# Optimization experiments

Hardware: AMD Instinct MI355X
Metric: run time of the kernel (lower is better)

## Reference

```python
import jax, jax.numpy as jnp
from jax import lax
import numpy as np

# label LUT: 36 raw labels -> 20 classes (from the module's labmap dict)
LUT = jnp.array(list(range(20)) + [1,2,3,4,5,6,7,8,9,10,14,15,16,17,18,19], dtype=jnp.int32)
R = 20  # kernel radius = ceil(truncated(4) * max sigma(5)); static for jit


def _gauss_kernel(sigma):
    k = jnp.arange(-R, R + 1, dtype=jnp.float32)
    w = jnp.exp(-0.5 * (k / sigma) ** 2)
    return w / jnp.sum(w)


def _smooth_axis(vol, w, axis):
    # vol: [D,H,W]; separable 1D zero-padded convolution along `axis`
    v = jnp.moveaxis(vol, axis, -1)
    sh = v.shape
    v2 = v.reshape(-1, 1, sh[-1])                      # [N,1,L]
    out = lax.conv_general_dilated(v2, w.reshape(1, 1, -1), (1,), [(R, R)])
    return jnp.moveaxis(out.reshape(sh), -1, axis)


def _gsmooth3(vol, sigma):
    # vol: [D,H,W]
    w = _gauss_kernel(sigma)
    for ax in range(3):
        vol = _smooth_axis(vol, w, ax)
    return vol


def setup_inputs() -> dict:
    key = jax.random.key(0)
    ks = jax.random.split(key, 6)
    shape = (1, 128, 160, 128)
    x = jax.random.randint(ks[0], shape, 0, 36, dtype=jnp.int32)
    noise = jax.random.normal(ks[1], (20,) + shape, dtype=jnp.float32)
    mus = jax.random.uniform(ks[2], (20,), minval=0.0, maxval=255.0, dtype=jnp.float32)
    stds = jax.random.uniform(ks[3], (20,), minval=0.0, maxval=16.0, dtype=jnp.float32)
    gmm_sigmas = jax.random.uniform(ks[4], (20,), minval=0.1, maxval=5.0, dtype=jnp.float32)
    final_sigma = jax.random.uniform(ks[5], (), minval=0.1, maxval=5.0, dtype=jnp.float32)
    return {"x": x, "noise": noise, "mus": mus, "stds": stds,
            "gmm_sigmas": gmm_sigmas, "final_sigma": final_sigma}


def reference(x, noise, mus, stds, gmm_sigmas, final_sigma):
    # 1) vectorized LUT remap (replaces the sequential tensor.apply_)
    xr = LUT[x[0]]                                      # [D,H,W] int32
    # 2) per-class masked Gaussian noise fields: (mu_i + std_i * N(0,1)) * (xr == i)
    classes = jnp.arange(20, dtype=jnp.int32)
    masks = (xr[None] == classes[:, None, None, None]).astype(jnp.float32)  # [20,D,H,W]
    fields = (mus[:, None, None, None] + stds[:, None, None, None] * noise[:, 0]) * masks
    # 3) per-class Gaussian smoothing (vmapped over the 20 classes), then sum
    smoothed = jax.vmap(_gsmooth3)(fields, gmm_sigmas)  # [20,D,H,W]
    summed = jnp.sum(smoothed, axis=0)                  # [D,H,W]
    # 4) final Gaussian smooth
    out = _gsmooth3(summed, final_sigma)
    return out[None]                                    # [1,D,H,W]
```

## Files before the change

kernel.cpp:

```cpp
#include <hip/hip_runtime.h>

constexpr int DD = 128, HH = 160, WW = 128;
constexpr int ZSTR = HH * WW;
constexpr long long NV = (long long)DD * HH * WW;
constexpr long long VOLB = NV * 4;
constexpr int RAD = 20, NTAP = 41;
constexpr int PW = 176;
constexpr int PADC = 24;
constexpr long long NVP = (long long)DD * HH * PW;

__device__ __forceinline__ int lutmap(int v) {
    return v < 20 ? v : (v < 30 ? v - 19 : v - 16);
}

__device__ __forceinline__ void taps(const float* win, const float* __restrict__ w,
                                     float acc[8]) {
#pragma unroll
    for (int k = 0; k < NTAP; ++k) {
        float wk = w[k];
#pragma unroll
        for (int p = 0; p < 8; ++p) acc[p] = fmaf(wk, win[k + p], acc[p]);
    }
}

__global__ __launch_bounds__(256) void kprep2(const int* __restrict__ x,
                                              const float* __restrict__ noise,
                                              const float* __restrict__ mus,
                                              const float* __restrict__ stds,
                                              float* __restrict__ vp,
                                              unsigned char* __restrict__ cp) {
    int z = blockIdx.y;
    int idx = blockIdx.x * 256 + threadIdx.x;
    int y = idx / PW, xp = idx - y * PW;
    long long po = (long long)z * HH * PW + idx;
    int gx = xp - PADC;
    if ((unsigned)gx < (unsigned)WW) {
        long long gi = (long long)z * ZSTR + (long long)y * WW + gx;
        int c = lutmap(x[gi]);
        vp[po] = mus[c] + stds[c] * noise[(long long)c * NV + gi];
        cp[po] = (unsigned char)c;
    } else {
        vp[po] = 0.f;
        cp[po] = (unsigned char)255;
    }
}

__global__ __launch_bounds__(256) void kpad(const float* __restrict__ src,
                                            float* __restrict__ vp) {
    int z = blockIdx.y;
    int idx = blockIdx.x * 256 + threadIdx.x;
    int y = idx / PW, xp = idx - y * PW;
    long long po = (long long)z * HH * PW + idx;
    int gx = xp - PADC;
    vp[po] = ((unsigned)gx < (unsigned)WW)
                 ? src[(long long)z * ZSTR + (long long)y * WW + gx]
                 : 0.f;
}

__global__ void kweights(const float* __restrict__ gsig, const float* __restrict__ fsig,
                         float* __restrict__ wts) {
    int c = threadIdx.x;
    if (c > 20) return;
    float sigma = (c < 20) ? gsig[c] : fsig[0];
    float inv = 1.0f / sigma;
    float buf[NTAP];
    float s = 0.f;
    for (int k = 0; k < NTAP; ++k) {
        float d = (float)(k - RAD) * inv;
        buf[k] = expf(-0.5f * d * d);
        s += buf[k];
    }
    float r = 1.0f / s;
    for (int k = 0; k < NTAP; ++k) wts[c * NTAP + k] = buf[k] * r;
}

template <bool MASKED>
__global__ __launch_bounds__(256, 4) void ksmooth_xy2(const float* __restrict__ vp,
                                                      const unsigned char* __restrict__ cp,
                                                      const float* __restrict__ wts,
                                                      float* __restrict__ dst, int c0) {
    __shared__ float A2[208][33];

    const int cls_i = MASKED ? (c0 + (int)blockIdx.x) : 20;
    const int x0 = (int)blockIdx.y * 32;
    const int z = blockIdx.z;
    const float* __restrict__ w = wts + cls_i * NTAP;
    const int tid = threadIdx.x;

    for (int i = tid; i < 48 * 32; i += 256) {
        int r = i >> 5, xx = i & 31;
        A2[(r < 24) ? r : (160 + r)][xx] = 0.f;
    }

    const long long zb = (long long)z * HH * PW;
    const int m = tid & 3, q = tid >> 2, xb = m * 8;
#pragma unroll
    for (int pass = 0; pass < 3; ++pass) {
        int y = pass * 64 + q;
        if (y < HH) {
            const float* srcp = vp + zb + (long long)y * PW + (x0 + xb + 4);
            float win[48];
            if (MASKED) {
                const unsigned* cu =
                    (const unsigned*)(cp + zb + (long long)y * PW + (x0 + xb + 4));
                const unsigned cb = (unsigned)cls_i;
#pragma unroll
                for (int i = 0; i < 12; ++i) {
                    float4 v4 = ((const float4*)srcp)[i];
                    unsigned u = cu[i];
                    win[4 * i + 0] = ((u & 0xffu) == cb) ? v4.x : 0.f;
                    win[4 * i + 1] = (((u >> 8) & 0xffu) == cb) ? v4.y : 0.f;
                    win[4 * i + 2] = (((u >> 16) & 0xffu) == cb) ? v4.z : 0.f;
                    win[4 * i + 3] = ((u >> 24) == cb) ? v4.w : 0.f;
                }
            } else {
#pragma unroll
                for (int i = 0; i < 12; ++i) {
                    float4 v4 = ((const float4*)srcp)[i];
                    win[4 * i + 0] = v4.x;
                    win[4 * i + 1] = v4.y;
                    win[4 * i + 2] = v4.z;
                    win[4 * i + 3] = v4.w;
                }
            }
            float acc[8] = {0, 0, 0, 0, 0, 0, 0, 0};
            taps(win, w, acc);
#pragma unroll
            for (int p = 0; p < 8; ++p) A2[24 + y][xb + p] = acc[p];
        }
    }
    __syncthreads();

    const int x = tid & 31, yg = tid >> 5;
    const long long obase =
        (MASKED ? ((long long)blockIdx.x * DD + z) : (long long)z) * ZSTR;
#pragma unroll
    for (int pass = 0; pass < 3; ++pass) {
        int yb = pass * 64 + yg * 8;
        if (yb < HH) {
            float win[48];
#pragma unroll
            for (int j = 0; j < 48; ++j) win[j] = A2[yb + 4 + j][x];
            float acc[8] = {0, 0, 0, 0, 0, 0, 0, 0};
            taps(win, w, acc);
#pragma unroll
            for (int p = 0; p < 8; ++p)
                dst[obase + (long long)(yb + p) * WW + x0 + x] = acc[p];
        }
    }
}

template <bool ACCUM>
__global__ __launch_bounds__(256) void ksmooth_z(const float* __restrict__ src,
                                                 const float* __restrict__ wts,
                                                 float* __restrict__ out, int c0,
                                                 int nc) {
    constexpr int LW = 33;
    __shared__ float L[104 * LW];

    const int x0 = blockIdx.x * 32;
    const int z0 = blockIdx.y * 64;
    const int y = blockIdx.z;
    const int x = threadIdx.x & 31;
    const int tg = threadIdx.x >> 5;

    float acc[8] = {0, 0, 0, 0, 0, 0, 0, 0};
    for (int cc = 0; cc < nc; ++cc) {
        const float* w = wts + (ACCUM ? (c0 + cc) : 20) * NTAP;
        const float* sv = src + (long long)cc * NV;
        for (int t = tg; t < 104; t += 8) {
            int gz = z0 - RAD + t;
            float v = ((unsigned)gz < (unsigned)DD)
                          ? sv[(long long)gz * ZSTR + (long long)y * WW + x0 + x]
                          : 0.f;
            L[t * LW + x] = v;
        }
        __syncthreads();
        {
            const int zb2 = tg * 8;
            float win[48];
#pragma unroll
            for (int j = 0; j < 48; ++j) win[j] = L[(zb2 + j) * LW + x];
            taps(win, w, acc);
        }
        __syncthreads();
    }
    const int zb2 = tg * 8;
#pragma unroll
    for (int p = 0; p < 8; ++p) {
        long long o = (long long)(z0 + zb2 + p) * ZSTR + (long long)y * WW + x0 + x;
        if (ACCUM)
            out[o] += acc[p];
        else
            out[o] = acc[p];
    }
}

extern "C" void kernel_launch(void* const* d_in, const int* in_sizes, int n_in,
                              void* d_out, int out_size, void* d_ws, size_t ws_size,
                              hipStream_t stream) {
    const int* x = (const int*)d_in[0];
    const float* noise = (const float*)d_in[1];
    const float* mus = (const float*)d_in[2];
    const float* stds = (const float*)d_in[3];
    const float* gsig = (const float*)d_in[4];
    const float* fsig = (const float*)d_in[5];
    float* out = (float*)d_out;

    char* ws = (char*)d_ws;
    size_t off = 0;
    float* wts = (float*)(ws + off);
    off += 4096;
    float* vp = (float*)(ws + off);
    off += (size_t)(NVP * 4);
    unsigned char* cpv = (unsigned char*)(ws + off);
    off += (size_t)NVP;
    float* xy = (float*)(ws + off);
    float* ftmp = xy;

    long long cap = ((long long)ws_size - (long long)off) / VOLB;
    int C = cap < 1 ? 1 : (cap > 20 ? 20 : (int)cap);

    kweights<<<1, 64, 0, stream>>>(gsig, fsig, wts);
    kprep2<<<dim3(HH * PW / 256, DD), 256, 0, stream>>>(x, noise, mus, stds, vp, cpv);
    hipMemsetAsync(d_out, 0, (size_t)VOLB, stream);

    for (int c0 = 0; c0 < 20; c0 += C) {
        int cc = (20 - c0) < C ? (20 - c0) : C;
        ksmooth_xy2<true><<<dim3(cc, 4, DD), 256, 0, stream>>>(vp, cpv, wts, xy, c0);
        ksmooth_z<true><<<dim3(4, 2, HH), 256, 0, stream>>>(xy, wts, out, c0, cc);
    }
    kpad<<<dim3(HH * PW / 256, DD), 256, 0, stream>>>(out, vp);
    ksmooth_xy2<false><<<dim3(1, 4, DD), 256, 0, stream>>>(vp, cpv, wts, ftmp, 0);
    ksmooth_z<false><<<dim3(4, 2, HH), 256, 0, stream>>>(ftmp, wts, out, 0, 1);
}
```

Measured before the change: 572.4 us.

## Rewrite z-smoothing with full-depth tiles, float4 loads and double-buffered class prefetch

The z-axis smoothing kernel now gives each block a 16-wide column spanning all 128 z slices, instead of a 32-wide column covering 64 z. This removes the 40-slice halo reload and the per-element bounds checks; the zero halos are written to shared memory once. Global loads become float4, and the next class's slab is prefetched into registers and written to a second shared buffer while the current class is convolved, dropping one barrier per class. The cost is larger shared-memory use per block, which may lower occupancy, and narrower 16-float output rows.

```diff
diff --git a/kernel.cpp b/kernel.cpp
--- a/kernel.cpp
+++ b/kernel.cpp
@@ -151,44 +151,81 @@
 }
 
 template <bool ACCUM>
-__global__ __launch_bounds__(256) void ksmooth_z(const float* __restrict__ src,
-                                                 const float* __restrict__ wts,
-                                                 float* __restrict__ out, int c0,
-                                                 int nc) {
-    constexpr int LW = 33;
-    __shared__ float L[104 * LW];
-
-    const int x0 = blockIdx.x * 32;
-    const int z0 = blockIdx.y * 64;
-    const int y = blockIdx.z;
-    const int x = threadIdx.x & 31;
-    const int tg = threadIdx.x >> 5;
+__global__ __launch_bounds__(256) void ksmooth_z3(const float* __restrict__ src,
+                                                  const float* __restrict__ wts,
+                                                  float* __restrict__ out, int c0,
+                                                  int nc) {
+    __shared__ float L[2][168][17];
+
+    const int x0 = (int)blockIdx.x * 16;
+    const int y = (int)blockIdx.y;
+    const int tid = threadIdx.x;
+    const int sxq = tid & 3;
+    const int szr = tid >> 2;
+    const int cx = tid & 15;
+    const int tg = tid >> 4;
+    const int zb = tg * 8;
+
+    const long long colbase = (long long)y * WW + x0;
+    const long long sgoff = colbase + sxq * 4;
+
+    for (int i = tid; i < 2 * 40 * 16; i += 256) {
+        int b = i / 640;
+        int rem = i - b * 640;
+        int r = rem >> 4, col = rem & 15;
+        L[b][(r < 20) ? r : (128 + r)][col] = 0.f;
+    }
+
+    {
+        const float4 va = *(const float4*)(src + (long long)szr * ZSTR + sgoff);
+        const float4 vb = *(const float4*)(src + (long long)(szr + 64) * ZSTR + sgoff);
+        const int wc = sxq * 4;
+        L[0][20 + szr][wc + 0] = va.x;
+        L[0][20 + szr][wc + 1] = va.y;
+        L[0][20 + szr][wc + 2] = va.z;
+        L[0][20 + szr][wc + 3] = va.w;
+        L[0][84 + szr][wc + 0] = vb.x;
+        L[0][84 + szr][wc + 1] = vb.y;
+        L[0][84 + szr][wc + 2] = vb.z;
+        L[0][84 + szr][wc + 3] = vb.w;
+    }
+    __syncthreads();
 
     float acc[8] = {0, 0, 0, 0, 0, 0, 0, 0};
     for (int cc = 0; cc < nc; ++cc) {
-        const float* w = wts + (ACCUM ? (c0 + cc) : 20) * NTAP;
-        const float* sv = src + (long long)cc * NV;
-        for (int t = tg; t < 104; t += 8) {
-            int gz = z0 - RAD + t;
-            float v = ((unsigned)gz < (unsigned)DD)
-                          ? sv[(long long)gz * ZSTR + (long long)y * WW + x0 + x]
-                          : 0.f;
-            L[t * LW + x] = v;
+        const int cur = cc & 1;
+        const bool more = (cc + 1 < nc);
+        float4 na, nb;
+        if (more) {
+            const float* sv = src + (long long)(cc + 1) * NV;
+            na = *(const float4*)(sv + (long long)szr * ZSTR + sgoff);
+            nb = *(const float4*)(sv + (long long)(szr + 64) * ZSTR + sgoff);
+        }
+        {
+            const float* w = wts + (ACCUM ? (c0 + cc) : 20) * NTAP;
+            float win[48];
+#pragma unroll
+            for (int j = 0; j < 48; ++j) win[j] = L[cur][zb + j][cx];
+            taps(win, w, acc);
+        }
+        if (more) {
+            const int nxt = cur ^ 1;
+            const int wc = sxq * 4;
+            L[nxt][20 + szr][wc + 0] = na.x;
+            L[nxt][20 + szr][wc + 1] = na.y;
+            L[nxt][20 + szr][wc + 2] = na.z;
+            L[nxt][20 + szr][wc + 3] = na.w;
+            L[nxt][84 + szr][wc + 0] = nb.x;
+            L[nxt][84 + szr][wc + 1] = nb.y;
+            L[nxt][84 + szr][wc + 2] = nb.z;
+            L[nxt][84 + szr][wc + 3] = nb.w;
         }
         __syncthreads();
-        {
-            const int zb2 = tg * 8;
-            float win[48];
-#pragma unroll
-            for (int j = 0; j < 48; ++j) win[j] = L[(zb2 + j) * LW + x];
-            taps(win, w, acc);
-        }
-        __syncthreads();
-    }
-    const int zb2 = tg * 8;
+    }
+
 #pragma unroll
     for (int p = 0; p < 8; ++p) {
-        long long o = (long long)(z0 + zb2 + p) * ZSTR + (long long)y * WW + x0 + x;
+        long long o = (long long)(zb + p) * ZSTR + colbase + cx;
         if (ACCUM)
             out[o] += acc[p];
         else
@@ -228,9 +265,9 @@
     for (int c0 = 0; c0 < 20; c0 += C) {
         int cc = (20 - c0) < C ? (20 - c0) : C;
         ksmooth_xy2<true><<<dim3(cc, 4, DD), 256, 0, stream>>>(vp, cpv, wts, xy, c0);
-        ksmooth_z<true><<<dim3(4, 2, HH), 256, 0, stream>>>(xy, wts, out, c0, cc);
+        ksmooth_z3<true><<<dim3(WW / 16, HH), 256, 0, stream>>>(xy, wts, out, c0, cc);
     }
     kpad<<<dim3(HH * PW / 256, DD), 256, 0, stream>>>(out, vp);
     ksmooth_xy2<false><<<dim3(1, 4, DD), 256, 0, stream>>>(vp, cpv, wts, ftmp, 0);
-    ksmooth_z<false><<<dim3(4, 2, HH), 256, 0, stream>>>(ftmp, wts, out, 0, 1);
-}
+    ksmooth_z3<false><<<dim3(WW / 16, HH), 256, 0, stream>>>(ftmp, wts, out, 0, 1);
+}
```

Result: faster. 535.1 us (-6.5%).
